# Kernel optimization log

Hardware: AMD Instinct MI355X
Metric: run time of the kernel (lower is better)

## Reference

```python
import jax, jax.numpy as jnp
import numpy as np

KERNEL = 3
STRIDE = 1
I_SIZE = 16
O_SIZE = 16
ROUTINGS = 3
EPS = 1e-9


def kernel_tile(x, k, s):
    # x: [B,H,W,C] -> [B,H',W',k*k,C] (im2col patch extraction, position-major axis 3)
    B, H, W, C = x.shape
    Hp = (H - k) // s + 1
    Wp = (W - k) // s + 1
    patches = [x[:, i:i + s * (Hp - 1) + 1:s, j:j + s * (Wp - 1) + 1:s, :]
               for i in range(k) for j in range(k)]
    return jnp.stack(patches, axis=3)


def em_routing(votes, i_act, beta_v, beta_a, iters):
    # votes: [B,H,W,I,O,16], i_act: [B,H,W,I]
    B, H, W, I, O, P = votes.shape
    rr = jnp.full((B, H, W, I, O, 1), 1.0 / O, dtype=votes.dtype)
    i_act = i_act[..., None, None]                 # [B,H,W,I,1,1]
    bv = beta_v.reshape(1, 1, 1, 1, O, 1)
    ba = beta_a.reshape(1, 1, 1, 1, O, 1)
    it_min, it_max = 1.0, min(iters, 3.0)
    o_mean = o_stdv = o_act = None
    for it in range(iters):
        inv_temp = it_min + (it_max - it_min) * it / max(1.0, iters - 1.0)
        # M-step
        rr_prime = rr * i_act                                        # [B,H,W,I,O,1]
        rr_sum = jnp.sum(rr_prime, axis=3, keepdims=True)            # [B,H,W,1,O,1]
        o_mean = jnp.sum(rr_prime * votes, axis=3, keepdims=True) / (rr_sum + EPS)
        o_stdv = jnp.sqrt(jnp.sum(rr_prime * (votes - o_mean) ** 2, axis=3, keepdims=True) / (rr_sum + EPS))
        o_cost = (bv + jnp.log(o_stdv + EPS)) * rr_sum               # [B,H,W,1,O,16]
        o_act = jax.nn.sigmoid(inv_temp * (ba - jnp.sum(o_cost, axis=-1, keepdims=True)))  # [B,H,W,1,O,1]
        # E-step
        if it < iters - 1:
            o_p = (-jnp.sum((votes - o_mean) ** 2 / (2.0 * o_stdv ** 2 + EPS), axis=-1, keepdims=True)
                   - jnp.sum(jnp.log(o_stdv + EPS), axis=-1, keepdims=True))  # [B,H,W,I,O,1]
            zz = jnp.log(o_act + EPS) + o_p
            rr = jax.nn.softmax(zz, axis=4)
    pose = jnp.squeeze(o_mean, axis=3)             # [B,H,W,O,16]
    act = jnp.squeeze(o_act, axis=(3, 5))          # [B,H,W,O]
    return pose, act


def setup_inputs() -> dict:
    key = jax.random.key(0)
    k1, k2, k3, k4, k5 = jax.random.split(key, 5)
    B, H, W = 8, 14, 14
    return {
        "inputs_pose": jax.random.normal(k1, (B, H, W, I_SIZE * 16), dtype=jnp.float32),
        "inputs_activation": jax.random.uniform(k2, (B, H, W, I_SIZE), dtype=jnp.float32),
        "w": jax.random.normal(k3, (KERNEL * KERNEL * I_SIZE, O_SIZE, 4, 4), dtype=jnp.float32) * 0.1,
        "beta_v": jax.random.normal(k4, (1, 1, 1, O_SIZE), dtype=jnp.float32),
        "beta_a": jax.random.normal(k5, (1, 1, 1, O_SIZE), dtype=jnp.float32),
    }


def reference(inputs_pose, inputs_activation, w, beta_v, beta_a):
    B = inputs_pose.shape[0]
    pose_size = 4
    # im2col tiling
    pose_t = kernel_tile(inputs_pose, KERNEL, STRIDE)        # [B,H',W',9,I*16]
    act_t = kernel_tile(inputs_activation, KERNEL, STRIDE)   # [B,H',W',9,I]
    Sp = act_t.shape[1]
    pose_t = pose_t.reshape(-1, KERNEL * KERNEL * I_SIZE, 16)           # [N, 9I, 16]
    act_t = act_t.reshape(B, Sp, Sp, KERNEL * KERNEL * I_SIZE)          # [B,H',W',9I]
    # batched pose transform: votes[n,i,o] = pose[n,i] (4x4) @ w[i,o] (4x4)
    pose4 = pose_t.reshape(-1, KERNEL * KERNEL * I_SIZE, 4, 4)
    votes = jnp.einsum('nipq,ioqr->niopr', pose4, w)                    # [N, 9I, O, 4, 4]
    votes = votes.reshape(B, Sp, Sp, KERNEL * KERNEL * I_SIZE, O_SIZE, 16)
    pose, activation = em_routing(votes, act_t, beta_v, beta_a, ROUTINGS)
    pose = pose.reshape(B, Sp, Sp, O_SIZE, pose_size, pose_size)
    return pose, activation
```

## Files before the change

kernel.cpp:

```cpp
#include <hip/hip_runtime.h>

#define EPSF 1e-9f

constexpr int I   = 144;
constexpr int IC  = 36;
constexpr int RT  = 148;
constexpr int SP  = 20;
constexpr int QS  = 20;

__device__ __forceinline__ float dpp_xor1(float x) {
    return __int_as_float(__builtin_amdgcn_update_dpp(0, __float_as_int(x), 0xB1, 0xF, 0xF, true));
}
__device__ __forceinline__ float dpp_xor2(float x) {
    return __int_as_float(__builtin_amdgcn_update_dpp(0, __float_as_int(x), 0x4E, 0xF, 0xF, true));
}
__device__ __forceinline__ float dpp_ror4(float x) {
    return __int_as_float(__builtin_amdgcn_update_dpp(0, __float_as_int(x), 0x124, 0xF, 0xF, true));
}
__device__ __forceinline__ float dpp_ror8(float x) {
    return __int_as_float(__builtin_amdgcn_update_dpp(0, __float_as_int(x), 0x128, 0xF, 0xF, true));
}
__device__ __forceinline__ float quad_sum(float x) {
    float y = x + dpp_xor1(x);
    return y + dpp_xor2(y);
}
__device__ __forceinline__ float quad_max(float x) {
    float y = fmaxf(x, dpp_xor1(x));
    return fmaxf(y, dpp_xor2(y));
}
__device__ __forceinline__ float row_sum16(float x) {
    float y = quad_sum(x);
    y += dpp_ror4(y);
    return y + dpp_ror8(y);
}
__device__ __forceinline__ float add_xor16(float x) {
#if __has_builtin(__builtin_amdgcn_permlane16_swap)
    auto r = __builtin_amdgcn_permlane16_swap(__float_as_int(x), __float_as_int(x), false, false);
    return __int_as_float(r[0]) + __int_as_float(r[1]);
#else
    return x + __shfl_xor(x, 16);
#endif
}
__device__ __forceinline__ float add_xor32(float x) {
#if __has_builtin(__builtin_amdgcn_permlane32_swap)
    auto r = __builtin_amdgcn_permlane32_swap(__float_as_int(x), __float_as_int(x), false, false);
    return __int_as_float(r[0]) + __int_as_float(r[1]);
#else
    return x + __shfl_xor(x, 32);
#endif
}
__device__ __forceinline__ float frcp(float x) { return __builtin_amdgcn_rcpf(x); }
__device__ __forceinline__ float flog2(float x) {
#if __has_builtin(__builtin_amdgcn_logf)
    return __builtin_amdgcn_logf(x);
#else
    return __log2f(x);
#endif
}
__device__ __forceinline__ float fexp2(float x) {
#if __has_builtin(__builtin_amdgcn_exp2f)
    return __builtin_amdgcn_exp2f(x);
#else
    return exp2f(x);
#endif
}

#define LN2F     0.69314718056f
#define INV_LN2F 1.44269504089f

__global__ void transpose_w_kernel(const float* __restrict__ w, float* __restrict__ wt) {
    const int i = blockIdx.x;
    const int t = threadIdx.x;
    const float val = w[i * 256 + t];
    const int o = t >> 4, q = (t >> 2) & 3, pc = t & 3;
    wt[i * 256 + o * 16 + pc * 4 + q] = val;
}

template <bool USE_WT>
__global__ __launch_bounds__(1024, 4)
void capsule_em_kernel(const float* __restrict__ pose_in,
                       const float* __restrict__ act_in,
                       const float* __restrict__ wmat,
                       const float* __restrict__ beta_v,
                       const float* __restrict__ beta_a,
                       float* __restrict__ out)
{
    __shared__ __align__(16) float s_pose[I * SP];
    __shared__ __align__(16) float s_zr[16 * RT];
    __shared__ __align__(16) float s_q[I * QS];
    __shared__ __align__(16) float s_iact[I + 4];
    __shared__ float s_Lo[16];

    const int tid  = threadIdx.x;
    const int o    = tid >> 6;
    const int lane = tid & 63;
    const int c    = lane >> 4;
    const int p    = lane & 15;
    const int pr   = p >> 2;
    const int pc   = p & 3;
    const int i0   = c * IC;
    const bool pb0 = pc & 1;
    const bool pb1 = pc & 2;

    const int n   = blockIdx.x;
    const int b   = n / 144;
    const int rem = n - b * 144;
    const int hp  = rem / 12;
    const int wp  = rem - hp * 12;

    if (tid < 576) {
        const int pk = tid >> 6, l6 = tid & 63;
        const int ki = pk / 3, kj = pk - ki * 3;
        const float4 val = *reinterpret_cast<const float4*>(
            &pose_in[((b * 14 + hp + ki) * 14 + (wp + kj)) * 256 + l6 * 4]);
        const int i = pk * 16 + (l6 >> 2), e = (l6 & 3) * 4;
        *reinterpret_cast<float4*>(&s_pose[i * SP + e]) = val;
    } else if (tid < 720) {
        const int t = tid - 576;
        const int pk = t >> 4, ic = t & 15;
        const int ki = pk / 3, kj = pk - ki * 3;
        s_iact[t] = act_in[((b * 14 + hp + ki) * 14 + (wp + kj)) * 16 + ic];
    }
    __syncthreads();

    float v[IC];
    #pragma unroll
    for (int ii = 0; ii < IC; ++ii) {
        const int i = i0 + ii;
        const float4 pv = *reinterpret_cast<const float4*>(&s_pose[i * SP + pr * 4]);
        if (USE_WT) {
            const float4 wv = *reinterpret_cast<const float4*>(&wmat[i * 256 + o * 16 + pc * 4]);
            v[ii] = pv.x * wv.x + pv.y * wv.y + pv.z * wv.z + pv.w * wv.w;
        } else {
            const float* wb = &wmat[i * 256 + o * 16 + pc];
            v[ii] = pv.x * wb[0] + pv.y * wb[4] + pv.z * wb[8] + pv.w * wb[12];
        }
    }

    const float bv = beta_v[o];
    const float ba = beta_a[o];

    float mean = 0.0f, o_act = 0.0f;

    #pragma unroll 1
    for (int it = 0; it < 3; ++it) {
        float accS = 0.0f, acc1 = 0.0f, acc2 = 0.0f;
        const float* rrow = (it == 0) ? &s_iact[i0] : &s_zr[o * RT + i0];
        #pragma unroll
        for (int jj = 0; jj < 9; ++jj) {
            const float4 r4 = *reinterpret_cast<const float4*>(&rrow[jj * 4]);
            const float r[4] = {r4.x, r4.y, r4.z, r4.w};
            #pragma unroll
            for (int k = 0; k < 4; ++k) {
                const float t = r[k] * v[jj * 4 + k];
                accS += r[k];
                acc1 += t;
                acc2 += t * v[jj * 4 + k];
            }
        }
        accS = add_xor16(accS); accS = add_xor32(accS);
        acc1 = add_xor16(acc1); acc1 = add_xor32(acc1);
        acc2 = add_xor16(acc2); acc2 = add_xor32(acc2);
        if (it == 0) {
            accS *= 0.0625f; acc1 *= 0.0625f; acc2 *= 0.0625f;
        }

        const float inv = frcp(accS + EPSF);
        mean = acc1 * inv;
        float var = (acc2 - 2.0f * mean * acc1 + mean * mean * accS) * inv;
        var = fmaxf(var, 0.0f);
        const float slog2 = row_sum16(0.5f * flog2(var + 1e-18f));

        const float cost_sum = accS * (16.0f * bv + LN2F * slog2);
        const float it2 = INV_LN2F * (1.0f + (float)it);
        o_act = frcp(1.0f + fexp2(-it2 * (ba - cost_sum)));

        if (it < 2) {
            const float a2  = INV_LN2F * frcp(2.0f * var + EPSF);
            const float b22 = 2.0f * mean * a2;
            const float cq2 = row_sum16(mean * mean * a2);
            const float Lo  = flog2(o_act + EPSF) - slog2 - cq2;
            if (lane == 0) s_Lo[o] = Lo;
            #pragma unroll
            for (int j = 0; j < 9; ++j) {
                float ct[4];
                #pragma unroll
                for (int t = 0; t < 4; ++t) {
                    const float vv = v[4 * j + t];
                    ct[t] = vv * fmaf(vv, a2, -b22);
                }
                const float k01 = pb0 ? ct[1] : ct[0];
                const float s01 = pb0 ? ct[0] : ct[1];
                const float k23 = pb0 ? ct[3] : ct[2];
                const float s23 = pb0 ? ct[2] : ct[3];
                const float a01 = k01 + dpp_xor1(s01);
                const float a23 = k23 + dpp_xor1(s23);
                const float kk  = pb1 ? a23 : a01;
                const float ss  = pb1 ? a01 : a23;
                const float qsum = kk + dpp_xor2(ss);
                float fs = qsum + dpp_ror4(qsum);
                fs += dpp_ror8(fs);
                if (pr == (j & 3))
                    s_q[(i0 + 4 * j + pc) * QS + o] = fs;
            }
            __syncthreads();
            if (tid < 576) {
                const int si = tid >> 2, sj = tid & 3;
                const float4 qv = *reinterpret_cast<const float4*>(&s_q[si * QS + sj * 4]);
                float zz[4];
                zz[0] = s_Lo[sj * 4 + 0] - qv.x;
                zz[1] = s_Lo[sj * 4 + 1] - qv.y;
                zz[2] = s_Lo[sj * 4 + 2] - qv.z;
                zz[3] = s_Lo[sj * 4 + 3] - qv.w;
                float m = fmaxf(fmaxf(zz[0], zz[1]), fmaxf(zz[2], zz[3]));
                m = quad_max(m);
                const float e0 = fexp2(zz[0] - m), e1 = fexp2(zz[1] - m);
                const float e2 = fexp2(zz[2] - m), e3 = fexp2(zz[3] - m);
                const float s = quad_sum(e0 + e1 + e2 + e3);
                const float sc = s_iact[si] * frcp(s);
                s_zr[(sj * 4 + 0) * RT + si] = e0 * sc;
                s_zr[(sj * 4 + 1) * RT + si] = e1 * sc;
                s_zr[(sj * 4 + 2) * RT + si] = e2 * sc;
                s_zr[(sj * 4 + 3) * RT + si] = e3 * sc;
            }
            __syncthreads();
        }
    }

    if (c == 0) out[n * 256 + o * 16 + p] = mean;
    if (lane == 0) out[8 * 12 * 12 * 256 + n * 16 + o] = o_act;
}

extern "C" void kernel_launch(void* const* d_in, const int* in_sizes, int n_in,
                              void* d_out, int out_size, void* d_ws, size_t ws_size,
                              hipStream_t stream) {
    const float* pose = (const float*)d_in[0];
    const float* act  = (const float*)d_in[1];
    const float* w    = (const float*)d_in[2];
    const float* bv   = (const float*)d_in[3];
    const float* ba   = (const float*)d_in[4];
    float* out = (float*)d_out;

    const size_t wt_bytes = size_t(I) * 256 * sizeof(float);
    if (ws_size >= wt_bytes) {
        float* wt = (float*)d_ws;
        transpose_w_kernel<<<dim3(I), dim3(256), 0, stream>>>(w, wt);
        capsule_em_kernel<true><<<dim3(1152), dim3(1024), 0, stream>>>(pose, act, wt, bv, ba, out);
    } else {
        capsule_em_kernel<false><<<dim3(1152), dim3(1024), 0, stream>>>(pose, act, w, bv, ba, out);
    }
}
```

Baseline: 111.5 us.

## Compute softmax redundantly per wave to drop a block barrier

Replaces the separate softmax phase, where 576 threads normalise across output capsules before a second __syncthreads, with a redundant per-wave computation. Each wave now reads all 16 output scores for its inputs from a transposed, double-buffered q table and writes only its own capsule's routing weight. This removes one block-wide barrier per routing iteration. The cost is roughly 16 times more exp2 work, extra shared-memory reads per wave, and more LDS for the double buffer, which may hurt occupancy.

```diff
diff --git a/kernel.cpp b/kernel.cpp
--- a/kernel.cpp
+++ b/kernel.cpp
@@ -6,7 +6,6 @@
 constexpr int IC  = 36;
 constexpr int RT  = 148;
 constexpr int SP  = 20;
-constexpr int QS  = 20;
 
 __device__ __forceinline__ float dpp_xor1(float x) {
     return __int_as_float(__builtin_amdgcn_update_dpp(0, __float_as_int(x), 0xB1, 0xF, 0xF, true));
@@ -23,10 +22,6 @@
 __device__ __forceinline__ float quad_sum(float x) {
     float y = x + dpp_xor1(x);
     return y + dpp_xor2(y);
-}
-__device__ __forceinline__ float quad_max(float x) {
-    float y = fmaxf(x, dpp_xor1(x));
-    return fmaxf(y, dpp_xor2(y));
 }
 __device__ __forceinline__ float row_sum16(float x) {
     float y = quad_sum(x);
@@ -87,9 +82,9 @@
 {
     __shared__ __align__(16) float s_pose[I * SP];
     __shared__ __align__(16) float s_zr[16 * RT];
-    __shared__ __align__(16) float s_q[I * QS];
+    __shared__ __align__(16) float s_qt[2][16 * RT];
     __shared__ __align__(16) float s_iact[I + 4];
-    __shared__ float s_Lo[16];
+    __shared__ __align__(16) float s_Lo[2][16];
 
     const int tid  = threadIdx.x;
     const int o    = tid >> 6;
@@ -180,7 +175,8 @@
             const float b22 = 2.0f * mean * a2;
             const float cq2 = row_sum16(mean * mean * a2);
             const float Lo  = flog2(o_act + EPSF) - slog2 - cq2;
-            if (lane == 0) s_Lo[o] = Lo;
+            float* const qt = &s_qt[it][0];
+            if (lane == 0) s_Lo[it][o] = Lo;
             #pragma unroll
             for (int j = 0; j < 9; ++j) {
                 float ct[4];
@@ -201,29 +197,41 @@
                 float fs = qsum + dpp_ror4(qsum);
                 fs += dpp_ror8(fs);
                 if (pr == (j & 3))
-                    s_q[(i0 + 4 * j + pc) * QS + o] = fs;
+                    qt[o * RT + (i0 + 4 * j + pc)] = fs;
             }
             __syncthreads();
-            if (tid < 576) {
-                const int si = tid >> 2, sj = tid & 3;
-                const float4 qv = *reinterpret_cast<const float4*>(&s_q[si * QS + sj * 4]);
-                float zz[4];
-                zz[0] = s_Lo[sj * 4 + 0] - qv.x;
-                zz[1] = s_Lo[sj * 4 + 1] - qv.y;
-                zz[2] = s_Lo[sj * 4 + 2] - qv.z;
-                zz[3] = s_Lo[sj * 4 + 3] - qv.w;
-                float m = fmaxf(fmaxf(zz[0], zz[1]), fmaxf(zz[2], zz[3]));
-                m = quad_max(m);
-                const float e0 = fexp2(zz[0] - m), e1 = fexp2(zz[1] - m);
-                const float e2 = fexp2(zz[2] - m), e3 = fexp2(zz[3] - m);
-                const float s = quad_sum(e0 + e1 + e2 + e3);
-                const float sc = s_iact[si] * frcp(s);
-                s_zr[(sj * 4 + 0) * RT + si] = e0 * sc;
-                s_zr[(sj * 4 + 1) * RT + si] = e1 * sc;
-                s_zr[(sj * 4 + 2) * RT + si] = e2 * sc;
-                s_zr[(sj * 4 + 3) * RT + si] = e3 * sc;
-            }
-            __syncthreads();
+
+            const float Lo_own = Lo;
+            float Lw[16];
+            #pragma unroll
+            for (int k4 = 0; k4 < 4; ++k4) {
+                const float4 l4 = *reinterpret_cast<const float4*>(&s_Lo[it][k4 * 4]);
+                Lw[k4 * 4 + 0] = l4.x; Lw[k4 * 4 + 1] = l4.y;
+                Lw[k4 * 4 + 2] = l4.z; Lw[k4 * 4 + 3] = l4.w;
+            }
+            #pragma unroll
+            for (int rpt = 0; rpt < 3; ++rpt) {
+                const int i = lane + 64 * rpt;
+                if (i < I) {
+                    float z[16];
+                    #pragma unroll
+                    for (int oo = 0; oo < 16; ++oo)
+                        z[oo] = Lw[oo] - qt[oo * RT + i];
+                    float m01 = fmaxf(z[0], z[1]),  m23 = fmaxf(z[2], z[3]);
+                    float m45 = fmaxf(z[4], z[5]),  m67 = fmaxf(z[6], z[7]);
+                    float m89 = fmaxf(z[8], z[9]),  mab = fmaxf(z[10], z[11]);
+                    float mcd = fmaxf(z[12], z[13]), mef = fmaxf(z[14], z[15]);
+                    const float m = fmaxf(fmaxf(fmaxf(m01, m23), fmaxf(m45, m67)),
+                                          fmaxf(fmaxf(m89, mab), fmaxf(mcd, mef)));
+                    float s = 0.0f;
+                    #pragma unroll
+                    for (int oo = 0; oo < 16; ++oo)
+                        s += fexp2(z[oo] - m);
+                    const float qown = qt[o * RT + i];
+                    const float rr = s_iact[i] * fexp2(Lo_own - qown - m) * frcp(s);
+                    s_zr[o * RT + i] = rr;
+                }
+            }
         }
     }
 
```

Measured after the change: 134.3 us. 20.4% more time.

## Halve block size so each wave handles two output capsules

Applied to the files above, without the earlier changes.

Shrinks the block from 1024 to 512 threads. Each wavefront now computes votes and EM statistics for two output capsules (o and o+8), with the loads and softmax passes rebalanced to match. The aim is more instruction-level parallelism per wave and less barrier cost per block. The trade-off is double the vote registers per thread (72 instead of 36), which may lower occupancy or cause spills.

```diff
diff --git a/kernel.cpp b/kernel.cpp
--- a/kernel.cpp
+++ b/kernel.cpp
@@ -77,7 +77,7 @@
 }
 
 template <bool USE_WT>
-__global__ __launch_bounds__(1024, 4)
+__global__ __launch_bounds__(512, 4)
 void capsule_em_kernel(const float* __restrict__ pose_in,
                        const float* __restrict__ act_in,
                        const float* __restrict__ wmat,
@@ -92,8 +92,10 @@
     __shared__ float s_Lo[16];
 
     const int tid  = threadIdx.x;
-    const int o    = tid >> 6;
+    const int wv   = tid >> 6;
     const int lane = tid & 63;
+    const int oa   = wv;
+    const int ob   = wv + 8;
     const int c    = lane >> 4;
     const int p    = lane & 15;
     const int pr   = p >> 2;
@@ -108,127 +110,185 @@
     const int hp  = rem / 12;
     const int wp  = rem - hp * 12;
 
-    if (tid < 576) {
-        const int pk = tid >> 6, l6 = tid & 63;
+    {
+        const int t0 = tid;
+        const int pk = t0 >> 6, l6 = t0 & 63;
         const int ki = pk / 3, kj = pk - ki * 3;
         const float4 val = *reinterpret_cast<const float4*>(
             &pose_in[((b * 14 + hp + ki) * 14 + (wp + kj)) * 256 + l6 * 4]);
         const int i = pk * 16 + (l6 >> 2), e = (l6 & 3) * 4;
         *reinterpret_cast<float4*>(&s_pose[i * SP + e]) = val;
-    } else if (tid < 720) {
-        const int t = tid - 576;
-        const int pk = t >> 4, ic = t & 15;
+    }
+    if (tid < 64) {
+        const int t1 = tid + 512;
+        const int pk = t1 >> 6, l6 = t1 & 63;
         const int ki = pk / 3, kj = pk - ki * 3;
-        s_iact[t] = act_in[((b * 14 + hp + ki) * 14 + (wp + kj)) * 16 + ic];
+        const float4 val = *reinterpret_cast<const float4*>(
+            &pose_in[((b * 14 + hp + ki) * 14 + (wp + kj)) * 256 + l6 * 4]);
+        const int i = pk * 16 + (l6 >> 2), e = (l6 & 3) * 4;
+        *reinterpret_cast<float4*>(&s_pose[i * SP + e]) = val;
+    }
+    if (tid < 144) {
+        const int pk = tid >> 4, ic = tid & 15;
+        const int ki = pk / 3, kj = pk - ki * 3;
+        s_iact[tid] = act_in[((b * 14 + hp + ki) * 14 + (wp + kj)) * 16 + ic];
     }
     __syncthreads();
 
-    float v[IC];
+    float va[IC], vb[IC];
     #pragma unroll
     for (int ii = 0; ii < IC; ++ii) {
         const int i = i0 + ii;
         const float4 pv = *reinterpret_cast<const float4*>(&s_pose[i * SP + pr * 4]);
         if (USE_WT) {
-            const float4 wv = *reinterpret_cast<const float4*>(&wmat[i * 256 + o * 16 + pc * 4]);
-            v[ii] = pv.x * wv.x + pv.y * wv.y + pv.z * wv.z + pv.w * wv.w;
+            const float4 wa = *reinterpret_cast<const float4*>(&wmat[i * 256 + oa * 16 + pc * 4]);
+            const float4 wb = *reinterpret_cast<const float4*>(&wmat[i * 256 + ob * 16 + pc * 4]);
+            va[ii] = pv.x * wa.x + pv.y * wa.y + pv.z * wa.z + pv.w * wa.w;
+            vb[ii] = pv.x * wb.x + pv.y * wb.y + pv.z * wb.z + pv.w * wb.w;
         } else {
-            const float* wb = &wmat[i * 256 + o * 16 + pc];
-            v[ii] = pv.x * wb[0] + pv.y * wb[4] + pv.z * wb[8] + pv.w * wb[12];
+            const float* wba = &wmat[i * 256 + oa * 16 + pc];
+            const float* wbb = &wmat[i * 256 + ob * 16 + pc];
+            va[ii] = pv.x * wba[0] + pv.y * wba[4] + pv.z * wba[8] + pv.w * wba[12];
+            vb[ii] = pv.x * wbb[0] + pv.y * wbb[4] + pv.z * wbb[8] + pv.w * wbb[12];
         }
     }
 
-    const float bv = beta_v[o];
-    const float ba = beta_a[o];
-
-    float mean = 0.0f, o_act = 0.0f;
+    const float bva = beta_v[oa], bvb = beta_v[ob];
+    const float baa = beta_a[oa], bab = beta_a[ob];
+
+    float mean_a = 0.0f, mean_b = 0.0f, oact_a = 0.0f, oact_b = 0.0f;
 
     #pragma unroll 1
     for (int it = 0; it < 3; ++it) {
-        float accS = 0.0f, acc1 = 0.0f, acc2 = 0.0f;
-        const float* rrow = (it == 0) ? &s_iact[i0] : &s_zr[o * RT + i0];
+        float aSa = 0.0f, a1a = 0.0f, a2a = 0.0f;
+        float aSb = 0.0f, a1b = 0.0f, a2b = 0.0f;
+        const float* rra = (it == 0) ? &s_iact[i0] : &s_zr[oa * RT + i0];
+        const float* rrb = (it == 0) ? &s_iact[i0] : &s_zr[ob * RT + i0];
         #pragma unroll
         for (int jj = 0; jj < 9; ++jj) {
-            const float4 r4 = *reinterpret_cast<const float4*>(&rrow[jj * 4]);
-            const float r[4] = {r4.x, r4.y, r4.z, r4.w};
+            const float4 r4a = *reinterpret_cast<const float4*>(&rra[jj * 4]);
+            const float4 r4b = *reinterpret_cast<const float4*>(&rrb[jj * 4]);
+            const float ra[4] = {r4a.x, r4a.y, r4a.z, r4a.w};
+            const float rb[4] = {r4b.x, r4b.y, r4b.z, r4b.w};
             #pragma unroll
             for (int k = 0; k < 4; ++k) {
-                const float t = r[k] * v[jj * 4 + k];
-                accS += r[k];
-                acc1 += t;
-                acc2 += t * v[jj * 4 + k];
+                const float ta = ra[k] * va[jj * 4 + k];
+                const float tb = rb[k] * vb[jj * 4 + k];
+                aSa += ra[k];  a1a += ta;  a2a += ta * va[jj * 4 + k];
+                aSb += rb[k];  a1b += tb;  a2b += tb * vb[jj * 4 + k];
             }
         }
-        accS = add_xor16(accS); accS = add_xor32(accS);
-        acc1 = add_xor16(acc1); acc1 = add_xor32(acc1);
-        acc2 = add_xor16(acc2); acc2 = add_xor32(acc2);
+        aSa = add_xor16(aSa); aSb = add_xor16(aSb);
+        a1a = add_xor16(a1a); a1b = add_xor16(a1b);
+        a2a = add_xor16(a2a); a2b = add_xor16(a2b);
+        aSa = add_xor32(aSa); aSb = add_xor32(aSb);
+        a1a = add_xor32(a1a); a1b = add_xor32(a1b);
+        a2a = add_xor32(a2a); a2b = add_xor32(a2b);
         if (it == 0) {
-            accS *= 0.0625f; acc1 *= 0.0625f; acc2 *= 0.0625f;
+            aSa *= 0.0625f; a1a *= 0.0625f; a2a *= 0.0625f;
+            aSb *= 0.0625f; a1b *= 0.0625f; a2b *= 0.0625f;
         }
 
-        const float inv = frcp(accS + EPSF);
-        mean = acc1 * inv;
-        float var = (acc2 - 2.0f * mean * acc1 + mean * mean * accS) * inv;
-        var = fmaxf(var, 0.0f);
-        const float slog2 = row_sum16(0.5f * flog2(var + 1e-18f));
-
-        const float cost_sum = accS * (16.0f * bv + LN2F * slog2);
+        const float inva = frcp(aSa + EPSF);
+        const float invb = frcp(aSb + EPSF);
+        mean_a = a1a * inva;
+        mean_b = a1b * invb;
+        float vara = (a2a - 2.0f * mean_a * a1a + mean_a * mean_a * aSa) * inva;
+        float varb = (a2b - 2.0f * mean_b * a1b + mean_b * mean_b * aSb) * invb;
+        vara = fmaxf(vara, 0.0f);
+        varb = fmaxf(varb, 0.0f);
+        const float sl2a = row_sum16(0.5f * flog2(vara + 1e-18f));
+        const float sl2b = row_sum16(0.5f * flog2(varb + 1e-18f));
+
+        const float csa = aSa * (16.0f * bva + LN2F * sl2a);
+        const float csb = aSb * (16.0f * bvb + LN2F * sl2b);
         const float it2 = INV_LN2F * (1.0f + (float)it);
-        o_act = frcp(1.0f + fexp2(-it2 * (ba - cost_sum)));
+        oact_a = frcp(1.0f + fexp2(-it2 * (baa - csa)));
+        oact_b = frcp(1.0f + fexp2(-it2 * (bab - csb)));
 
         if (it < 2) {
-            const float a2  = INV_LN2F * frcp(2.0f * var + EPSF);
-            const float b22 = 2.0f * mean * a2;
-            const float cq2 = row_sum16(mean * mean * a2);
-            const float Lo  = flog2(o_act + EPSF) - slog2 - cq2;
-            if (lane == 0) s_Lo[o] = Lo;
+            const float a2fa = INV_LN2F * frcp(2.0f * vara + EPSF);
+            const float a2fb = INV_LN2F * frcp(2.0f * varb + EPSF);
+            const float b2a  = 2.0f * mean_a * a2fa;
+            const float b2b  = 2.0f * mean_b * a2fb;
+            const float cqa  = row_sum16(mean_a * mean_a * a2fa);
+            const float cqb  = row_sum16(mean_b * mean_b * a2fb);
+            const float LoA  = flog2(oact_a + EPSF) - sl2a - cqa;
+            const float LoB  = flog2(oact_b + EPSF) - sl2b - cqb;
+            if (lane == 0) { s_Lo[oa] = LoA; s_Lo[ob] = LoB; }
             #pragma unroll
             for (int j = 0; j < 9; ++j) {
-                float ct[4];
+                float cta[4], ctb[4];
                 #pragma unroll
                 for (int t = 0; t < 4; ++t) {
-                    const float vv = v[4 * j + t];
-                    ct[t] = vv * fmaf(vv, a2, -b22);
+                    const float v1 = va[4 * j + t];
+                    const float v2 = vb[4 * j + t];
+                    cta[t] = v1 * fmaf(v1, a2fa, -b2a);
+                    ctb[t] = v2 * fmaf(v2, a2fb, -b2b);
                 }
-                const float k01 = pb0 ? ct[1] : ct[0];
-                const float s01 = pb0 ? ct[0] : ct[1];
-                const float k23 = pb0 ? ct[3] : ct[2];
-                const float s23 = pb0 ? ct[2] : ct[3];
-                const float a01 = k01 + dpp_xor1(s01);
-                const float a23 = k23 + dpp_xor1(s23);
-                const float kk  = pb1 ? a23 : a01;
-                const float ss  = pb1 ? a01 : a23;
-                const float qsum = kk + dpp_xor2(ss);
-                float fs = qsum + dpp_ror4(qsum);
-                fs += dpp_ror8(fs);
-                if (pr == (j & 3))
-                    s_q[(i0 + 4 * j + pc) * QS + o] = fs;
+                const float k01a = pb0 ? cta[1] : cta[0];
+                const float s01a = pb0 ? cta[0] : cta[1];
+                const float k23a = pb0 ? cta[3] : cta[2];
+                const float s23a = pb0 ? cta[2] : cta[3];
+                const float k01b = pb0 ? ctb[1] : ctb[0];
+                const float s01b = pb0 ? ctb[0] : ctb[1];
+                const float k23b = pb0 ? ctb[3] : ctb[2];
+                const float s23b = pb0 ? ctb[2] : ctb[3];
+                const float a01a = k01a + dpp_xor1(s01a);
+                const float a23a = k23a + dpp_xor1(s23a);
+                const float a01b = k01b + dpp_xor1(s01b);
+                const float a23b = k23b + dpp_xor1(s23b);
+                const float kka = pb1 ? a23a : a01a;
+                const float ssa = pb1 ? a01a : a23a;
+                const float kkb = pb1 ? a23b : a01b;
+                const float ssb = pb1 ? a01b : a23b;
+                const float qa = kka + dpp_xor2(ssa);
+                const float qb = kkb + dpp_xor2(ssb);
+                float fsa = qa + dpp_ror4(qa);
+                float fsb = qb + dpp_ror4(qb);
+                fsa += dpp_ror8(fsa);
+                fsb += dpp_ror8(fsb);
+                if (pr == (j & 3)) {
+                    s_q[(i0 + 4 * j + pc) * QS + oa] = fsa;
+                    s_q[(i0 + 4 * j + pc) * QS + ob] = fsb;
+                }
             }
             __syncthreads();
-            if (tid < 576) {
-                const int si = tid >> 2, sj = tid & 3;
-                const float4 qv = *reinterpret_cast<const float4*>(&s_q[si * QS + sj * 4]);
-                float zz[4];
-                zz[0] = s_Lo[sj * 4 + 0] - qv.x;
-                zz[1] = s_Lo[sj * 4 + 1] - qv.y;
-                zz[2] = s_Lo[sj * 4 + 2] - qv.z;
-                zz[3] = s_Lo[sj * 4 + 3] - qv.w;
-                float m = fmaxf(fmaxf(zz[0], zz[1]), fmaxf(zz[2], zz[3]));
-                m = quad_max(m);
-                const float e0 = fexp2(zz[0] - m), e1 = fexp2(zz[1] - m);
-                const float e2 = fexp2(zz[2] - m), e3 = fexp2(zz[3] - m);
-                const float s = quad_sum(e0 + e1 + e2 + e3);
-                const float sc = s_iact[si] * frcp(s);
-                s_zr[(sj * 4 + 0) * RT + si] = e0 * sc;
-                s_zr[(sj * 4 + 1) * RT + si] = e1 * sc;
-                s_zr[(sj * 4 + 2) * RT + si] = e2 * sc;
-                s_zr[(sj * 4 + 3) * RT + si] = e3 * sc;
+            #pragma unroll
+            for (int pass = 0; pass < 2; ++pass) {
+                const int item = tid + pass * 512;
+                if (pass == 0 || tid < 64) {
+                    const int si = item >> 2, sj = item & 3;
+                    const float4 qv = *reinterpret_cast<const float4*>(&s_q[si * QS + sj * 4]);
+                    float zz[4];
+                    zz[0] = s_Lo[sj * 4 + 0] - qv.x;
+                    zz[1] = s_Lo[sj * 4 + 1] - qv.y;
+                    zz[2] = s_Lo[sj * 4 + 2] - qv.z;
+                    zz[3] = s_Lo[sj * 4 + 3] - qv.w;
+                    float m = fmaxf(fmaxf(zz[0], zz[1]), fmaxf(zz[2], zz[3]));
+                    m = quad_max(m);
+                    const float e0 = fexp2(zz[0] - m), e1 = fexp2(zz[1] - m);
+                    const float e2 = fexp2(zz[2] - m), e3 = fexp2(zz[3] - m);
+                    const float s = quad_sum(e0 + e1 + e2 + e3);
+                    const float sc = s_iact[si] * frcp(s);
+                    s_zr[(sj * 4 + 0) * RT + si] = e0 * sc;
+                    s_zr[(sj * 4 + 1) * RT + si] = e1 * sc;
+                    s_zr[(sj * 4 + 2) * RT + si] = e2 * sc;
+                    s_zr[(sj * 4 + 3) * RT + si] = e3 * sc;
+                }
             }
             __syncthreads();
         }
     }
 
-    if (c == 0) out[n * 256 + o * 16 + p] = mean;
-    if (lane == 0) out[8 * 12 * 12 * 256 + n * 16 + o] = o_act;
+    if (c == 0) {
+        out[n * 256 + oa * 16 + p] = mean_a;
+        out[n * 256 + ob * 16 + p] = mean_b;
+    }
+    if (lane == 0) {
+        out[8 * 12 * 12 * 256 + n * 16 + oa] = oact_a;
+        out[8 * 12 * 12 * 256 + n * 16 + ob] = oact_b;
+    }
 }
 
 extern "C" void kernel_launch(void* const* d_in, const int* in_sizes, int n_in,
@@ -245,8 +305,8 @@
     if (ws_size >= wt_bytes) {
         float* wt = (float*)d_ws;
         transpose_w_kernel<<<dim3(I), dim3(256), 0, stream>>>(w, wt);
-        capsule_em_kernel<true><<<dim3(1152), dim3(1024), 0, stream>>>(pose, act, wt, bv, ba, out);
+        capsule_em_kernel<true><<<dim3(1152), dim3(512), 0, stream>>>(pose, act, wt, bv, ba, out);
     } else {
-        capsule_em_kernel<false><<<dim3(1152), dim3(1024), 0, stream>>>(pose, act, w, bv, ba, out);
-    }
-}
+        capsule_em_kernel<false><<<dim3(1152), dim3(512), 0, stream>>>(pose, act, w, bv, ba, out);
+    }
+}
```

After: 108.3 us (median of 3 runs). -2.9%, faster.
